# Performance work log

Hardware: AMD Instinct MI355X
Metric: run time of the kernel (lower is better)

Reference implementation:

```python
import jax, jax.numpy as jnp
import numpy as np

PAD_VALUE = 0.0


def setup_inputs() -> dict:
    key = jax.random.key(0)
    k1, k2 = jax.random.split(key)
    B, T, D = 32, 512, 384
    xs = jax.random.normal(k1, (B, T, D), dtype=jnp.float32)
    ds = jax.random.randint(k2, (B, T), 0, 8, dtype=jnp.int32)
    return {"xs": xs, "ds": ds, "max_frame": 4096}


def reference(xs, ds, max_frame):
    """LengthRegulator forward (alpha == 1.0).

    xs: (B, T, D) float token embeddings
    ds: (B, T) int durations (zero-duration tokens are skipped)
    max_frame: python int; output is padded/stacked to (B, max_frame, D)
    """
    B, T, D = xs.shape
    cum = jnp.cumsum(ds, axis=1)                      # (B, T) exclusive-end offsets
    total = cum[:, -1]                                # (B,) total frames per sequence
    t = jnp.arange(max_frame, dtype=cum.dtype)        # (F,)
    # token index producing frame t: first i with cum[i] > t (skips d==0 tokens)
    idx = jax.vmap(lambda c: jnp.searchsorted(c, t, side="right"))(cum)  # (B, F)
    idx = jnp.minimum(idx, T - 1)
    out = jnp.take_along_axis(xs, idx[:, :, None], axis=1)               # (B, F, D)
    valid = (t[None, :] < total[:, None])[:, :, None]                    # (B, F, 1)
    return jnp.where(valid, out, jnp.asarray(PAD_VALUE, xs.dtype))
```

## Files before the change

kernel.cpp:

```cpp
#include <hip/hip_runtime.h>
#include <hip/hip_bf16.h>

constexpr int B     = 32;
constexpr int T     = 512;
constexpr int D     = 384;
constexpr int MF    = 4096;
constexpr int D4    = D / 4;
constexpr int CHUNK = 64;
constexpr int BLOCK = 256;
constexpr int ITERS = CHUNK * D4 / BLOCK;

typedef float f32x4 __attribute__((ext_vector_type(4)));

__global__ __launch_bounds__(BLOCK) void lr_fused(const float* __restrict__ xs,
                                                  const int* __restrict__ ds,
                                                  float* __restrict__ out) {
    const int b    = blockIdx.y;
    const int base = blockIdx.x * CHUNK;
    const int tid  = threadIdx.x;

    __shared__ int cum[T];
    __shared__ int map_l[CHUNK];

    cum[tid]         = ds[b * T + tid];
    cum[tid + BLOCK] = ds[b * T + tid + BLOCK];
    __syncthreads();
    #pragma unroll
    for (int off = 1; off <= BLOCK; off <<= 1) {
        const int v0 = (tid >= off) ? cum[tid - off] : 0;
        const int v1 = cum[tid + BLOCK - off];
        __syncthreads();
        cum[tid]         += v0;
        cum[tid + BLOCK] += v1;
        __syncthreads();
    }
    const int total = cum[T - 1];

    if (tid < CHUNK) {
        const int f = base + tid;
        int m = -1;
        if (f < total) {
            int lo = 0, hi = T;
            while (lo < hi) {
                const int mid = (lo + hi) >> 1;
                if (cum[mid] <= f) lo = mid + 1; else hi = mid;
            }
            m = lo;
        }
        map_l[tid] = m;
    }
    __syncthreads();

    const f32x4* __restrict__ xs4 = (const f32x4*)(xs) + (size_t)b * T * D4;
    f32x4* __restrict__ out4 = (f32x4*)(out) + ((size_t)b * MF + base) * D4;

    int f = tid / D4;
    int q = tid - f * D4;
    int o = tid;
    #pragma unroll 4
    for (int it = 0; it < ITERS; ++it) {
        const int tok = map_l[f];
        f32x4 v = {0.f, 0.f, 0.f, 0.f};
        if (tok >= 0) v = xs4[tok * D4 + q];
        out4[o] = v;
        f += 2; q += 64; o += BLOCK;
        if (q >= D4) { q -= D4; ++f; }
    }
}

extern "C" void kernel_launch(void* const* d_in, const int* in_sizes, int n_in,
                              void* d_out, int out_size, void* d_ws, size_t ws_size,
                              hipStream_t stream) {
    const float* xs = (const float*)d_in[0];
    const int*   ds = (const int*)d_in[1];

    float* out = (float*)d_out;

    dim3 grid(MF / CHUNK, B);
    lr_fused<<<grid, BLOCK, 0, stream>>>(xs, ds, out);
}
```

Baseline: 37.71 us.

## Replace shared-memory scan and binary search with wave-shuffle scan and range scatter

The block-wide Hillis-Steele prefix sum over shared memory needed about twenty barriers. It is replaced by a per-wave shuffle scan over pairs of durations, with wave totals combined through a small shared array. Each thread then writes its two tokens' frame ranges directly into the chunk's frame-to-token map, instead of each frame binary-searching the cumulative array. This shortens the per-block prologue so the memory-bound copy phase starts sooner. Threads whose tokens have long durations do a short serial scatter loop.

```diff
diff --git a/kernel.cpp b/kernel.cpp
--- a/kernel.cpp
+++ b/kernel.cpp
@@ -18,36 +18,38 @@
     const int b    = blockIdx.y;
     const int base = blockIdx.x * CHUNK;
     const int tid  = threadIdx.x;
+    const int lane = tid & 63;
+    const int wv   = tid >> 6;
 
-    __shared__ int cum[T];
+    __shared__ int wtot[4];
     __shared__ int map_l[CHUNK];
 
-    cum[tid]         = ds[b * T + tid];
-    cum[tid + BLOCK] = ds[b * T + tid + BLOCK];
+    if (tid < CHUNK) map_l[tid] = -1;
+
+    const int2 dp = ((const int2*)(ds + b * T))[tid];
+    int inc = dp.x + dp.y;
+    #pragma unroll
+    for (int off = 1; off < 64; off <<= 1) {
+        const int v = __shfl_up(inc, off);
+        if (lane >= off) inc += v;
+    }
+    if (lane == 63) wtot[wv] = inc;
     __syncthreads();
+
+    int wpre = 0;
     #pragma unroll
-    for (int off = 1; off <= BLOCK; off <<= 1) {
-        const int v0 = (tid >= off) ? cum[tid - off] : 0;
-        const int v1 = cum[tid + BLOCK - off];
-        __syncthreads();
-        cum[tid]         += v0;
-        cum[tid + BLOCK] += v1;
-        __syncthreads();
-    }
-    const int total = cum[T - 1];
+    for (int w = 0; w < 3; ++w) wpre += (w < wv) ? wtot[w] : 0;
 
-    if (tid < CHUNK) {
-        const int f = base + tid;
-        int m = -1;
-        if (f < total) {
-            int lo = 0, hi = T;
-            while (lo < hi) {
-                const int mid = (lo + hi) >> 1;
-                if (cum[mid] <= f) lo = mid + 1; else hi = mid;
-            }
-            m = lo;
-        }
-        map_l[tid] = m;
+    const int incl = inc + wpre;
+    const int ex1  = incl - dp.y;
+    const int ex0  = ex1 - dp.x;
+
+    {
+        const int lo = base, hi = base + CHUNK;
+        const int s0 = max(ex0, lo), e0 = min(ex1, hi);
+        for (int i = s0; i < e0; ++i) map_l[i - lo] = 2 * tid;
+        const int s1 = max(ex1, lo), e1 = min(incl, hi);
+        for (int i = s1; i < e1; ++i) map_l[i - lo] = 2 * tid + 1;
     }
     __syncthreads();
 
```

Measured after the change: 36.65 us. 1.03x faster.
